# Kernel tuning notes

Hardware: AMD Instinct MI355X
Metric: run time of the kernel (lower is better)

The kernel has to match this reference:

```python
import jax, jax.numpy as jnp
import numpy as np

N_NODES = 50000
N_EDGES = 800000
D = 128


def setup_inputs() -> dict:
    key = jax.random.key(0)
    k1, k2, k3, k4, k5 = jax.random.split(key, 5)
    feature = jax.random.normal(k1, (N_NODES, D), dtype=jnp.float32)
    src = jax.random.randint(k2, (N_EDGES,), 0, N_NODES, dtype=jnp.int64)
    dst = jax.random.randint(k3, (N_EDGES,), 0, N_NODES, dtype=jnp.int64)
    # Linear(in_feats=128, out_feats=128) params
    W = jax.random.normal(k4, (D, D), dtype=jnp.float32) * (1.0 / np.sqrt(D))
    b = jax.random.normal(k5, (D,), dtype=jnp.float32) * 0.01
    return {"feature": feature, "src": src, "dst": dst, "W": W, "b": b}


def reference(feature, src, dst, W, b):
    n = feature.shape[0]
    # copy_src message: each edge carries h[src]; segment-mean over in-edges at dst
    msgs = feature[src]                                      # [E, D] irregular gather
    summed = jax.ops.segment_sum(msgs, dst, num_segments=n)  # [N, D] scatter-add
    cnt = jax.ops.segment_sum(jnp.ones((src.shape[0],), dtype=feature.dtype),
                              dst, num_segments=n)           # in-degree per node
    h = summed / jnp.clip(cnt, 1.0)[:, None]                 # mean (isolated nodes -> 0)
    # NodeApplyModule: ReLU(W h + b)
    return jax.nn.relu(h @ W.T + b)
```

## Files before the change

### kernel.cpp

```cpp
#include <hip/hip_runtime.h>

#define NN 50000
#define NE 800000
#define DD 128
#define NPAD 50176


__global__ __launch_bounds__(256) void k_hist(const int* __restrict__ dst,
                                              int* __restrict__ cnt) {
  int e = blockIdx.x * 256 + threadIdx.x;
  if (e < NE) atomicAdd(&cnt[dst[e]], 1);
}

__global__ __launch_bounds__(1024) void k_scan1(const int* __restrict__ cnt,
                                                int* __restrict__ pos) {
  __shared__ int sh[1024];
  int t = threadIdx.x;
  int base = t * 49;
  int ssum = 0;
  for (int i = 0; i < 49; ++i) ssum += cnt[base + i];
  sh[t] = ssum;
  __syncthreads();
  for (int o = 1; o < 1024; o <<= 1) {
    int x = (t >= o) ? sh[t - o] : 0;
    __syncthreads();
    sh[t] += x;
    __syncthreads();
  }
  int run = sh[t] - ssum;
  for (int i = 0; i < 49; ++i) {
    int v = cnt[base + i];
    pos[base + i] = run;
    run += v;
  }
}

__global__ __launch_bounds__(256) void k_fill(const int* __restrict__ src,
                                              const int* __restrict__ dst,
                                              int* __restrict__ pos,
                                              int* __restrict__ csr) {
  int e = blockIdx.x * 256 + threadIdx.x;
  if (e < NE) {
    int d = dst[e];
    int p = atomicAdd(&pos[d], 1);
    csr[p] = src[e];
  }
}

#define FMA8(R, H)                                          \
  {                                                         \
    acc[R][0] += (H)*w0.x; acc[R][1] += (H)*w0.y;           \
    acc[R][2] += (H)*w0.z; acc[R][3] += (H)*w0.w;           \
    acc[R][4] += (H)*w1.x; acc[R][5] += (H)*w1.y;           \
    acc[R][6] += (H)*w1.z; acc[R][7] += (H)*w1.w;           \
  }

__global__ __launch_bounds__(256) void k_gemmT(const float* __restrict__ feat,
                                               const float* __restrict__ W,
                                               float* __restrict__ g) {
  __shared__ float fs[32][260];
  __shared__ float ws[32][132];
  int tid = threadIdx.x;
  int row0 = blockIdx.x * 256;
  int tc = tid & 15;
  int tr = tid >> 4;
  float acc[16][8] = {};

  for (int kc = 0; kc < 4; ++kc) {
    if (kc) __syncthreads();
    for (int i = 0; i < 8; ++i) {
      int fidx = tid + (i << 8);
      int r = fidx >> 3;
      int q = fidx & 7;
      int grow = row0 + r;
      float4 v = make_float4(0.f, 0.f, 0.f, 0.f);
      if (grow < NN) v = ((const float4*)feat)[grow * 32 + kc * 8 + q];
      int k = q << 2;
      fs[k + 0][r] = v.x;
      fs[k + 1][r] = v.y;
      fs[k + 2][r] = v.z;
      fs[k + 3][r] = v.w;
    }
    for (int i = 0; i < 4; ++i) {
      int fidx = tid + (i << 8);
      int c = fidx >> 3;
      int q = fidx & 7;
      float4 v = ((const float4*)W)[c * 32 + kc * 8 + q];
      int k = q << 2;
      ws[k + 0][c] = v.x;
      ws[k + 1][c] = v.y;
      ws[k + 2][c] = v.z;
      ws[k + 3][c] = v.w;
    }
    __syncthreads();

#pragma unroll 8
    for (int k = 0; k < 32; ++k) {
      float4 w0 = *(const float4*)&ws[k][tc * 8];
      float4 w1 = *(const float4*)&ws[k][tc * 8 + 4];
      float4 h0 = *(const float4*)&fs[k][tr * 16];
      float4 h1 = *(const float4*)&fs[k][tr * 16 + 4];
      float4 h2 = *(const float4*)&fs[k][tr * 16 + 8];
      float4 h3 = *(const float4*)&fs[k][tr * 16 + 12];
      FMA8(0, h0.x) FMA8(1, h0.y) FMA8(2, h0.z) FMA8(3, h0.w)
      FMA8(4, h1.x) FMA8(5, h1.y) FMA8(6, h1.z) FMA8(7, h1.w)
      FMA8(8, h2.x) FMA8(9, h2.y) FMA8(10, h2.z) FMA8(11, h2.w)
      FMA8(12, h3.x) FMA8(13, h3.y) FMA8(14, h3.z) FMA8(15, h3.w)
    }
  }

#pragma unroll
  for (int r = 0; r < 16; ++r) {
    int grow = row0 + tr * 16 + r;
    if (grow < NN) {
      float4 o0, o1;
      o0.x = acc[r][0]; o0.y = acc[r][1]; o0.z = acc[r][2]; o0.w = acc[r][3];
      o1.x = acc[r][4]; o1.y = acc[r][5]; o1.z = acc[r][6]; o1.w = acc[r][7];
      float4* gp = (float4*)(g + (long long)grow * DD) + tc * 2;
      gp[0] = o0;
      gp[1] = o1;
    }
  }
}

__global__ __launch_bounds__(256) void k_gmean(const float* __restrict__ g,
                                               const int* __restrict__ csr,
                                               const int* __restrict__ pos,
                                               const int* __restrict__ cnt,
                                               const float* __restrict__ bias,
                                               float* __restrict__ out) {
  int n = blockIdx.x * 4 + (threadIdx.x >> 6);
  int lane = threadIdx.x & 63;
  int half = lane >> 5;
  int l32 = lane & 31;
  int end = pos[n];
  int c = cnt[n];
  float4 a = make_float4(0.f, 0.f, 0.f, 0.f);
  for (int base = end - c; base < end; base += 64) {
    int m = end - base;
    if (m > 64) m = 64;
    int s = (base + lane < end) ? csr[base + lane] : 0;
    for (int j = 0; j < m; j += 8) {
#pragma unroll
      for (int u = 0; u < 4; ++u) {
        int j2 = j + 2 * u + half;
        int sj = __shfl(s, j2);
        if (j2 < m) {
          float4 v = ((const float4*)(g + (long long)sj * DD))[l32];
          a.x += v.x; a.y += v.y; a.z += v.z; a.w += v.w;
        }
      }
    }
  }
  a.x += __shfl_xor(a.x, 32);
  a.y += __shfl_xor(a.y, 32);
  a.z += __shfl_xor(a.z, 32);
  a.w += __shfl_xor(a.w, 32);
  if (half == 0) {
    float inv = 1.0f / fmaxf((float)c, 1.0f);
    float4 b4 = ((const float4*)bias)[l32];
    float4 o;
    o.x = fmaxf(a.x * inv + b4.x, 0.f);
    o.y = fmaxf(a.y * inv + b4.y, 0.f);
    o.z = fmaxf(a.z * inv + b4.z, 0.f);
    o.w = fmaxf(a.w * inv + b4.w, 0.f);
    ((float4*)(out + (long long)n * DD))[l32] = o;
  }
}

__global__ __launch_bounds__(256) void k_gather_sum(const float* __restrict__ feat,
                                                    const int* __restrict__ csr,
                                                    const int* __restrict__ pos,
                                                    const int* __restrict__ cnt,
                                                    float* __restrict__ sum) {
  int n = blockIdx.x * 4 + (threadIdx.x >> 6);
  int lane = threadIdx.x & 63;
  int end = pos[n];
  int c = cnt[n];
  float ax = 0.f, ay = 0.f;
  for (int base = end - c; base < end; base += 64) {
    int m = end - base;
    if (m > 64) m = 64;
    int s = (base + lane < end) ? csr[base + lane] : 0;
    int j = 0;
    for (; j + 3 < m; j += 4) {
      int s0 = __shfl(s, j), s1 = __shfl(s, j + 1);
      int s2 = __shfl(s, j + 2), s3 = __shfl(s, j + 3);
      float2 v0 = ((const float2*)(feat + (long long)s0 * DD))[lane];
      float2 v1 = ((const float2*)(feat + (long long)s1 * DD))[lane];
      float2 v2 = ((const float2*)(feat + (long long)s2 * DD))[lane];
      float2 v3 = ((const float2*)(feat + (long long)s3 * DD))[lane];
      ax += (v0.x + v1.x) + (v2.x + v3.x);
      ay += (v0.y + v1.y) + (v2.y + v3.y);
    }
    for (; j < m; ++j) {
      int sj = __shfl(s, j);
      float2 v = ((const float2*)(feat + (long long)sj * DD))[lane];
      ax += v.x;
      ay += v.y;
    }
  }
  float2 o;
  o.x = ax;
  o.y = ay;
  ((float2*)(sum + (long long)n * DD))[lane] = o;
}

__global__ __launch_bounds__(256) void k_gemm_inplace(float* __restrict__ io,
                                                      const int* __restrict__ cnt,
                                                      const float* __restrict__ W,
                                                      const float* __restrict__ bias) {
  __shared__ float Wt[64][132];
  __shared__ __attribute__((aligned(16))) float hs[64][72];
  int tid = threadIdx.x;
  int row0 = blockIdx.x * 64;
  int tc = tid & 31;
  int tr = tid >> 5;
  float acc[8][4] = {};
  for (int p = 0; p < 2; ++p) {
    if (p) __syncthreads();
    for (int i = 0; i < 8; ++i) {
      int fidx = tid + (i << 8);
      int c = fidx >> 4;
      int kq = fidx & 15;
      float4 w = ((const float4*)W)[c * 32 + p * 16 + kq];
      int kk = kq << 2;
      Wt[kk + 0][c ^ (((kk + 0) & 31) << 2)] = w.x;
      Wt[kk + 1][c ^ (((kk + 1) & 31) << 2)] = w.y;
      Wt[kk + 2][c ^ (((kk + 2) & 31) << 2)] = w.z;
      Wt[kk + 3][c ^ (((kk + 3) & 31) << 2)] = w.w;
    }
    for (int i = 0; i < 4; ++i) {
      int fidx = tid + (i << 8);
      int r = fidx & 63;
      int kq = fidx >> 6;
      int grow = row0 + r;
      float4 v = make_float4(0.f, 0.f, 0.f, 0.f);
      if (grow < NN) {
        v = ((const float4*)io)[(long long)grow * 32 + p * 16 + kq];
        float inv = 1.0f / fmaxf((float)cnt[grow], 1.0f);
        v.x *= inv; v.y *= inv; v.z *= inv; v.w *= inv;
      }
      int kk = kq << 2;
      hs[kk + 0][r] = v.x;
      hs[kk + 1][r] = v.y;
      hs[kk + 2][r] = v.z;
      hs[kk + 3][r] = v.w;
    }
    __syncthreads();
#pragma unroll 4
    for (int kk = 0; kk < 64; ++kk) {
      float4 w4 = *(const float4*)&Wt[kk][(tc << 2) ^ ((kk & 31) << 2)];
      float4 h0 = *(const float4*)&hs[kk][tr << 3];
      float4 h1 = *(const float4*)&hs[kk][(tr << 3) + 4];
      acc[0][0] += h0.x * w4.x; acc[0][1] += h0.x * w4.y; acc[0][2] += h0.x * w4.z; acc[0][3] += h0.x * w4.w;
      acc[1][0] += h0.y * w4.x; acc[1][1] += h0.y * w4.y; acc[1][2] += h0.y * w4.z; acc[1][3] += h0.y * w4.w;
      acc[2][0] += h0.z * w4.x; acc[2][1] += h0.z * w4.y; acc[2][2] += h0.z * w4.z; acc[2][3] += h0.z * w4.w;
      acc[3][0] += h0.w * w4.x; acc[3][1] += h0.w * w4.y; acc[3][2] += h0.w * w4.z; acc[3][3] += h0.w * w4.w;
      acc[4][0] += h1.x * w4.x; acc[4][1] += h1.x * w4.y; acc[4][2] += h1.x * w4.z; acc[4][3] += h1.x * w4.w;
      acc[5][0] += h1.y * w4.x; acc[5][1] += h1.y * w4.y; acc[5][2] += h1.y * w4.z; acc[5][3] += h1.y * w4.w;
      acc[6][0] += h1.z * w4.x; acc[6][1] += h1.z * w4.y; acc[6][2] += h1.z * w4.z; acc[6][3] += h1.z * w4.w;
      acc[7][0] += h1.w * w4.x; acc[7][1] += h1.w * w4.y; acc[7][2] += h1.w * w4.z; acc[7][3] += h1.w * w4.w;
    }
  }
  float4 b4 = ((const float4*)bias)[tc];
#pragma unroll
  for (int r = 0; r < 8; ++r) {
    int row = row0 + (tr << 3) + r;
    if (row < NN) {
      float4 o;
      o.x = fmaxf(acc[r][0] + b4.x, 0.f);
      o.y = fmaxf(acc[r][1] + b4.y, 0.f);
      o.z = fmaxf(acc[r][2] + b4.z, 0.f);
      o.w = fmaxf(acc[r][3] + b4.w, 0.f);
      ((float4*)(io + (long long)row * DD))[tc] = o;
    }
  }
}

extern "C" void kernel_launch(void* const* d_in, const int* in_sizes, int n_in,
                              void* d_out, int out_size, void* d_ws, size_t ws_size,
                              hipStream_t stream) {
  const float* feature = (const float*)d_in[0];
  const int*   src     = (const int*)d_in[1];
  const int*   dst     = (const int*)d_in[2];
  const float* W       = (const float*)d_in[3];
  const float* bias    = (const float*)d_in[4];
  float* out = (float*)d_out;

  int* cnt = (int*)d_ws;
  int* pos = cnt + NPAD;
  int* csr = pos + NPAD;
  float* g = (float*)(csr + NE);

  size_t need_csr = (size_t)(2 * NPAD + NE) * sizeof(int);
  size_t need_g = need_csr + (size_t)NN * DD * sizeof(float);
  int nblk_e = (NE + 255) / 256;

  hipMemsetAsync(cnt, 0, NPAD * sizeof(int), stream);
  hipLaunchKernelGGL(k_hist, dim3(nblk_e), dim3(256), 0, stream, dst, cnt);
  hipLaunchKernelGGL(k_scan1, dim3(1), dim3(1024), 0, stream, cnt, pos);
  hipLaunchKernelGGL(k_fill, dim3(nblk_e), dim3(256), 0, stream, src, dst, pos, csr);

  if (ws_size >= need_g) {
    hipLaunchKernelGGL(k_gemmT, dim3((NN + 255) / 256), dim3(256), 0, stream,
                       feature, W, g);
    hipLaunchKernelGGL(k_gmean, dim3(NN / 4), dim3(256), 0, stream,
                       g, csr, pos, cnt, bias, out);
  } else {
    hipLaunchKernelGGL(k_gather_sum, dim3(NN / 4), dim3(256), 0, stream,
                       feature, csr, pos, cnt, out);
    hipLaunchKernelGGL(k_gemm_inplace, dim3((NN + 63) / 64), dim3(256), 0,
                       stream, out, cnt, W, bias);
  }
}
```

Baseline: 278.9 us.

## Fuse histogram into GEMM launch, parallelize scan, vectorize fill and gather

Runs the dst histogram in extra blocks of the GEMM launch so both share one kernel, with the GEMM retiled to 128x64 outputs per 128-thread block. The single-block scan becomes a 49-block scan whose block offsets are recomputed in each consumer. The CSR fill now reads int4 vectors of edges, and the gather-mean uses 32-lane half-waves with float4 loads, eight loads in flight and four accumulators. The aim is to remove the serial scan bottleneck and a launch, and to raise memory-level parallelism in the gather. In exchange, every fill and gather block repeats a small prefix over the block sums.

```diff
diff --git a/kernel.cpp b/kernel.cpp
--- a/kernel.cpp
+++ b/kernel.cpp
@@ -4,122 +4,155 @@
 #define NE 800000
 #define DD 128
 #define NPAD 50176
-
-
-__global__ __launch_bounds__(256) void k_hist(const int* __restrict__ dst,
-                                              int* __restrict__ cnt) {
-  int e = blockIdx.x * 256 + threadIdx.x;
-  if (e < NE) atomicAdd(&cnt[dst[e]], 1);
-}
-
-__global__ __launch_bounds__(1024) void k_scan1(const int* __restrict__ cnt,
-                                                int* __restrict__ pos) {
-  __shared__ int sh[1024];
-  int t = threadIdx.x;
-  int base = t * 49;
-  int ssum = 0;
-  for (int i = 0; i < 49; ++i) ssum += cnt[base + i];
-  sh[t] = ssum;
-  __syncthreads();
-  for (int o = 1; o < 1024; o <<= 1) {
-    int x = (t >= o) ? sh[t - o] : 0;
-    __syncthreads();
-    sh[t] += x;
-    __syncthreads();
-  }
-  int run = sh[t] - ssum;
-  for (int i = 0; i < 49; ++i) {
-    int v = cnt[base + i];
-    pos[base + i] = run;
-    run += v;
-  }
-}
-
-__global__ __launch_bounds__(256) void k_fill(const int* __restrict__ src,
-                                              const int* __restrict__ dst,
-                                              int* __restrict__ pos,
-                                              int* __restrict__ csr) {
-  int e = blockIdx.x * 256 + threadIdx.x;
-  if (e < NE) {
-    int d = dst[e];
-    int p = atomicAdd(&pos[d], 1);
-    csr[p] = src[e];
-  }
-}
-
-#define FMA8(R, H)                                          \
-  {                                                         \
-    acc[R][0] += (H)*w0.x; acc[R][1] += (H)*w0.y;           \
-    acc[R][2] += (H)*w0.z; acc[R][3] += (H)*w0.w;           \
-    acc[R][4] += (H)*w1.x; acc[R][5] += (H)*w1.y;           \
-    acc[R][6] += (H)*w1.z; acc[R][7] += (H)*w1.w;           \
-  }
-
-__global__ __launch_bounds__(256) void k_gemmT(const float* __restrict__ feat,
-                                               const float* __restrict__ W,
-                                               float* __restrict__ g) {
-  __shared__ float fs[32][260];
-  __shared__ float ws[32][132];
+#define NSB 49
+#define GB 784
+#define HB 782
+
+
+#define ACC4(A, V) { A.x += V.x; A.y += V.y; A.z += V.z; A.w += V.w; }
+
+#define BSUM_PREFIX(bsum, sbase)                                   \
+  {                                                                \
+    int tt = threadIdx.x;                                          \
+    if (tt < 64) {                                                 \
+      int b = (tt < NSB) ? bsum[tt] : 0;                           \
+      int z = b;                                                   \
+      _Pragma("unroll") for (int o = 1; o < 64; o <<= 1) {         \
+        int w_ = __shfl_up(z, o);                                  \
+        if (tt >= o) z += w_;                                      \
+      }                                                            \
+      sbase[tt] = z - b;                                           \
+    }                                                              \
+    __syncthreads();                                               \
+  }
+
+__global__ __launch_bounds__(128) void k_gemm_hist(
+    const float* __restrict__ feat, const float* __restrict__ W,
+    float* __restrict__ g, const int* __restrict__ dst, int* __restrict__ cnt) {
+  __shared__ float fs[32][132];
+  __shared__ float ws[32][68];
   int tid = threadIdx.x;
-  int row0 = blockIdx.x * 256;
-  int tc = tid & 15;
-  int tr = tid >> 4;
-  float acc[16][8] = {};
+  int bid = blockIdx.x;
+
+  if (bid >= GB) {
+    int idx = (bid - GB) * 128 + tid;
+    if (idx < NE / 8) {
+      const int4* d4 = (const int4*)dst;
+      int4 a = d4[idx * 2];
+      int4 b = d4[idx * 2 + 1];
+      atomicAdd(&cnt[a.x], 1); atomicAdd(&cnt[a.y], 1);
+      atomicAdd(&cnt[a.z], 1); atomicAdd(&cnt[a.w], 1);
+      atomicAdd(&cnt[b.x], 1); atomicAdd(&cnt[b.y], 1);
+      atomicAdd(&cnt[b.z], 1); atomicAdd(&cnt[b.w], 1);
+    }
+    return;
+  }
+
+  int row0 = (bid >> 1) * 128;
+  int col0 = (bid & 1) * 64;
+  int tc = tid & 7;
+  int trb = tid >> 3;
+  int wbase = tc * 8 + ((tc >> 2) << 2);
+  float acc[8][8] = {};
 
   for (int kc = 0; kc < 4; ++kc) {
     if (kc) __syncthreads();
     for (int i = 0; i < 8; ++i) {
-      int fidx = tid + (i << 8);
-      int r = fidx >> 3;
-      int q = fidx & 7;
+      int fidx = tid + (i << 7);
+      int r = fidx >> 3, q = fidx & 7;
       int grow = row0 + r;
       float4 v = make_float4(0.f, 0.f, 0.f, 0.f);
       if (grow < NN) v = ((const float4*)feat)[grow * 32 + kc * 8 + q];
       int k = q << 2;
-      fs[k + 0][r] = v.x;
-      fs[k + 1][r] = v.y;
-      fs[k + 2][r] = v.z;
-      fs[k + 3][r] = v.w;
+      fs[k][r] = v.x; fs[k + 1][r] = v.y; fs[k + 2][r] = v.z; fs[k + 3][r] = v.w;
     }
     for (int i = 0; i < 4; ++i) {
-      int fidx = tid + (i << 8);
-      int c = fidx >> 3;
-      int q = fidx & 7;
-      float4 v = ((const float4*)W)[c * 32 + kc * 8 + q];
+      int fidx = tid + (i << 7);
+      int c = fidx >> 3, q = fidx & 7;
+      float4 v = ((const float4*)W)[(col0 + c) * 32 + kc * 8 + q];
+      int sc = c + ((c >> 5) << 2);
       int k = q << 2;
-      ws[k + 0][c] = v.x;
-      ws[k + 1][c] = v.y;
-      ws[k + 2][c] = v.z;
-      ws[k + 3][c] = v.w;
+      ws[k][sc] = v.x; ws[k + 1][sc] = v.y; ws[k + 2][sc] = v.z; ws[k + 3][sc] = v.w;
     }
     __syncthreads();
+
+#define FM8(R, H)                                                       \
+    { acc[R][0] += (H)*w0.x; acc[R][1] += (H)*w0.y;                     \
+      acc[R][2] += (H)*w0.z; acc[R][3] += (H)*w0.w;                     \
+      acc[R][4] += (H)*w1.x; acc[R][5] += (H)*w1.y;                     \
+      acc[R][6] += (H)*w1.z; acc[R][7] += (H)*w1.w; }
 
 #pragma unroll 8
     for (int k = 0; k < 32; ++k) {
-      float4 w0 = *(const float4*)&ws[k][tc * 8];
-      float4 w1 = *(const float4*)&ws[k][tc * 8 + 4];
-      float4 h0 = *(const float4*)&fs[k][tr * 16];
-      float4 h1 = *(const float4*)&fs[k][tr * 16 + 4];
-      float4 h2 = *(const float4*)&fs[k][tr * 16 + 8];
-      float4 h3 = *(const float4*)&fs[k][tr * 16 + 12];
-      FMA8(0, h0.x) FMA8(1, h0.y) FMA8(2, h0.z) FMA8(3, h0.w)
-      FMA8(4, h1.x) FMA8(5, h1.y) FMA8(6, h1.z) FMA8(7, h1.w)
-      FMA8(8, h2.x) FMA8(9, h2.y) FMA8(10, h2.z) FMA8(11, h2.w)
-      FMA8(12, h3.x) FMA8(13, h3.y) FMA8(14, h3.z) FMA8(15, h3.w)
+      float4 w0 = *(const float4*)&ws[k][wbase];
+      float4 w1 = *(const float4*)&ws[k][wbase + 4];
+      float4 h0 = *(const float4*)&fs[k][trb * 8];
+      float4 h1 = *(const float4*)&fs[k][trb * 8 + 4];
+      FM8(0, h0.x) FM8(1, h0.y) FM8(2, h0.z) FM8(3, h0.w)
+      FM8(4, h1.x) FM8(5, h1.y) FM8(6, h1.z) FM8(7, h1.w)
     }
   }
 
 #pragma unroll
-  for (int r = 0; r < 16; ++r) {
-    int grow = row0 + tr * 16 + r;
+  for (int r = 0; r < 8; ++r) {
+    int grow = row0 + trb * 8 + r;
     if (grow < NN) {
       float4 o0, o1;
       o0.x = acc[r][0]; o0.y = acc[r][1]; o0.z = acc[r][2]; o0.w = acc[r][3];
       o1.x = acc[r][4]; o1.y = acc[r][5]; o1.z = acc[r][6]; o1.w = acc[r][7];
-      float4* gp = (float4*)(g + (long long)grow * DD) + tc * 2;
+      float4* gp = (float4*)(g + (size_t)grow * DD + col0) + tc * 2;
       gp[0] = o0;
       gp[1] = o1;
     }
+  }
+}
+
+__global__ __launch_bounds__(1024) void k_scan(const int* __restrict__ cnt,
+                                               int* __restrict__ pos,
+                                               int* __restrict__ bsum) {
+  __shared__ int wsum[16];
+  int t = threadIdx.x;
+  int gidx = blockIdx.x * 1024 + t;
+  int v = cnt[gidx];
+  int x = v;
+#pragma unroll
+  for (int o = 1; o < 64; o <<= 1) {
+    int y = __shfl_up(x, o);
+    if ((t & 63) >= o) x += y;
+  }
+  if ((t & 63) == 63) wsum[t >> 6] = x;
+  __syncthreads();
+  if (t < 64) {
+    int y = (t < 16) ? wsum[t] : 0;
+    int z = y;
+#pragma unroll
+    for (int o = 1; o < 16; o <<= 1) {
+      int w = __shfl_up(z, o);
+      if (t >= o) z += w;
+    }
+    if (t < 16) wsum[t] = z - y;
+  }
+  __syncthreads();
+  pos[gidx] = wsum[t >> 6] + x - v;
+  if (t == 1023) bsum[blockIdx.x] = wsum[15] + x;
+}
+
+__global__ __launch_bounds__(256) void k_fill(const int* __restrict__ src,
+                                              const int* __restrict__ dst,
+                                              int* __restrict__ pos,
+                                              int* __restrict__ csr,
+                                              const int* __restrict__ bsum) {
+  __shared__ int sbase[64];
+  BSUM_PREFIX(bsum, sbase)
+  int idx = blockIdx.x * 256 + threadIdx.x;
+  if (idx < NE / 4) {
+    int4 d = ((const int4*)dst)[idx];
+    int4 s = ((const int4*)src)[idx];
+    int p;
+    p = atomicAdd(&pos[d.x], 1); csr[sbase[d.x >> 10] + p] = s.x;
+    p = atomicAdd(&pos[d.y], 1); csr[sbase[d.y >> 10] + p] = s.y;
+    p = atomicAdd(&pos[d.z], 1); csr[sbase[d.z >> 10] + p] = s.z;
+    p = atomicAdd(&pos[d.w], 1); csr[sbase[d.w >> 10] + p] = s.w;
   }
 }
 
@@ -127,83 +160,101 @@
                                                const int* __restrict__ csr,
                                                const int* __restrict__ pos,
                                                const int* __restrict__ cnt,
+                                               const int* __restrict__ bsum,
                                                const float* __restrict__ bias,
                                                float* __restrict__ out) {
-  int n = blockIdx.x * 4 + (threadIdx.x >> 6);
-  int lane = threadIdx.x & 63;
-  int half = lane >> 5;
-  int l32 = lane & 31;
-  int end = pos[n];
+  __shared__ int sbase[64];
+  BSUM_PREFIX(bsum, sbase)
+  int tid = threadIdx.x;
+  int hw = tid >> 5, l32 = tid & 31;
+  int n = blockIdx.x * 8 + hw;
   int c = cnt[n];
-  float4 a = make_float4(0.f, 0.f, 0.f, 0.f);
-  for (int base = end - c; base < end; base += 64) {
-    int m = end - base;
-    if (m > 64) m = 64;
-    int s = (base + lane < end) ? csr[base + lane] : 0;
-    for (int j = 0; j < m; j += 8) {
-#pragma unroll
-      for (int u = 0; u < 4; ++u) {
-        int j2 = j + 2 * u + half;
-        int sj = __shfl(s, j2);
-        if (j2 < m) {
-          float4 v = ((const float4*)(g + (long long)sj * DD))[l32];
-          a.x += v.x; a.y += v.y; a.z += v.z; a.w += v.w;
-        }
-      }
-    }
-  }
-  a.x += __shfl_xor(a.x, 32);
-  a.y += __shfl_xor(a.y, 32);
-  a.z += __shfl_xor(a.z, 32);
-  a.w += __shfl_xor(a.w, 32);
-  if (half == 0) {
-    float inv = 1.0f / fmaxf((float)c, 1.0f);
-    float4 b4 = ((const float4*)bias)[l32];
-    float4 o;
-    o.x = fmaxf(a.x * inv + b4.x, 0.f);
-    o.y = fmaxf(a.y * inv + b4.y, 0.f);
-    o.z = fmaxf(a.z * inv + b4.z, 0.f);
-    o.w = fmaxf(a.w * inv + b4.w, 0.f);
-    ((float4*)(out + (long long)n * DD))[l32] = o;
-  }
-}
-
-__global__ __launch_bounds__(256) void k_gather_sum(const float* __restrict__ feat,
-                                                    const int* __restrict__ csr,
-                                                    const int* __restrict__ pos,
-                                                    const int* __restrict__ cnt,
-                                                    float* __restrict__ sum) {
-  int n = blockIdx.x * 4 + (threadIdx.x >> 6);
-  int lane = threadIdx.x & 63;
-  int end = pos[n];
+  int endg = sbase[n >> 10] + pos[n];
+  int start = endg - c;
+  float4 a0 = make_float4(0.f, 0.f, 0.f, 0.f), a1 = a0, a2 = a0, a3 = a0;
+
+  for (int base = start; base < endg; base += 32) {
+    int m = endg - base;
+    if (m > 32) m = 32;
+    int s = (l32 < m) ? csr[base + l32] : 0;
+    int j = 0;
+    for (; j + 8 <= m; j += 8) {
+      int s0 = __shfl(s, j + 0, 32), s1 = __shfl(s, j + 1, 32),
+          s2 = __shfl(s, j + 2, 32), s3 = __shfl(s, j + 3, 32),
+          s4 = __shfl(s, j + 4, 32), s5 = __shfl(s, j + 5, 32),
+          s6 = __shfl(s, j + 6, 32), s7 = __shfl(s, j + 7, 32);
+      float4 v0 = ((const float4*)(g + (size_t)s0 * DD))[l32];
+      float4 v1 = ((const float4*)(g + (size_t)s1 * DD))[l32];
+      float4 v2 = ((const float4*)(g + (size_t)s2 * DD))[l32];
+      float4 v3 = ((const float4*)(g + (size_t)s3 * DD))[l32];
+      float4 v4 = ((const float4*)(g + (size_t)s4 * DD))[l32];
+      float4 v5 = ((const float4*)(g + (size_t)s5 * DD))[l32];
+      float4 v6 = ((const float4*)(g + (size_t)s6 * DD))[l32];
+      float4 v7 = ((const float4*)(g + (size_t)s7 * DD))[l32];
+      ACC4(a0, v0) ACC4(a1, v1) ACC4(a2, v2) ACC4(a3, v3)
+      ACC4(a0, v4) ACC4(a1, v5) ACC4(a2, v6) ACC4(a3, v7)
+    }
+    for (; j < m; ++j) {
+      int sj = __shfl(s, j, 32);
+      float4 v = ((const float4*)(g + (size_t)sj * DD))[l32];
+      ACC4(a0, v)
+    }
+  }
+  a0.x += a1.x + a2.x + a3.x;
+  a0.y += a1.y + a2.y + a3.y;
+  a0.z += a1.z + a2.z + a3.z;
+  a0.w += a1.w + a2.w + a3.w;
+  float inv = 1.0f / fmaxf((float)c, 1.0f);
+  float4 b4 = ((const float4*)bias)[l32];
+  float4 o;
+  o.x = fmaxf(a0.x * inv + b4.x, 0.f);
+  o.y = fmaxf(a0.y * inv + b4.y, 0.f);
+  o.z = fmaxf(a0.z * inv + b4.z, 0.f);
+  o.w = fmaxf(a0.w * inv + b4.w, 0.f);
+  ((float4*)(out + (size_t)n * DD))[l32] = o;
+}
+
+__global__ __launch_bounds__(128) void k_hist(const int* __restrict__ dst,
+                                              int* __restrict__ cnt) {
+  int idx = blockIdx.x * 128 + threadIdx.x;
+  if (idx < NE / 8) {
+    const int4* d4 = (const int4*)dst;
+    int4 a = d4[idx * 2];
+    int4 b = d4[idx * 2 + 1];
+    atomicAdd(&cnt[a.x], 1); atomicAdd(&cnt[a.y], 1);
+    atomicAdd(&cnt[a.z], 1); atomicAdd(&cnt[a.w], 1);
+    atomicAdd(&cnt[b.x], 1); atomicAdd(&cnt[b.y], 1);
+    atomicAdd(&cnt[b.z], 1); atomicAdd(&cnt[b.w], 1);
+  }
+}
+
+__global__ __launch_bounds__(256) void k_gsum(const float* __restrict__ feat,
+                                              const int* __restrict__ csr,
+                                              const int* __restrict__ pos,
+                                              const int* __restrict__ cnt,
+                                              const int* __restrict__ bsum,
+                                              float* __restrict__ out) {
+  __shared__ int sbase[64];
+  BSUM_PREFIX(bsum, sbase)
+  int tid = threadIdx.x;
+  int hw = tid >> 5, l32 = tid & 31;
+  int n = blockIdx.x * 8 + hw;
   int c = cnt[n];
-  float ax = 0.f, ay = 0.f;
-  for (int base = end - c; base < end; base += 64) {
-    int m = end - base;
-    if (m > 64) m = 64;
-    int s = (base + lane < end) ? csr[base + lane] : 0;
-    int j = 0;
-    for (; j + 3 < m; j += 4) {
-      int s0 = __shfl(s, j), s1 = __shfl(s, j + 1);
-      int s2 = __shfl(s, j + 2), s3 = __shfl(s, j + 3);
-      float2 v0 = ((const float2*)(feat + (long long)s0 * DD))[lane];
-      float2 v1 = ((const float2*)(feat + (long long)s1 * DD))[lane];
-      float2 v2 = ((const float2*)(feat + (long long)s2 * DD))[lane];
-      float2 v3 = ((const float2*)(feat + (long long)s3 * DD))[lane];
-      ax += (v0.x + v1.x) + (v2.x + v3.x);
-      ay += (v0.y + v1.y) + (v2.y + v3.y);
-    }
-    for (; j < m; ++j) {
-      int sj = __shfl(s, j);
-      float2 v = ((const float2*)(feat + (long long)sj * DD))[lane];
-      ax += v.x;
-      ay += v.y;
-    }
-  }
-  float2 o;
-  o.x = ax;
-  o.y = ay;
-  ((float2*)(sum + (long long)n * DD))[lane] = o;
+  int endg = sbase[n >> 10] + pos[n];
+  int start = endg - c;
+  float4 a0 = make_float4(0.f, 0.f, 0.f, 0.f), a1 = a0;
+  for (int base = start; base < endg; base += 32) {
+    int m = endg - base;
+    if (m > 32) m = 32;
+    int s = (l32 < m) ? csr[base + l32] : 0;
+    for (int j = 0; j < m; ++j) {
+      int sj = __shfl(s, j, 32);
+      float4 v = ((const float4*)(feat + (size_t)sj * DD))[l32];
+      if (j & 1) { ACC4(a1, v) } else { ACC4(a0, v) }
+    }
+  }
+  a0.x += a1.x; a0.y += a1.y; a0.z += a1.z; a0.w += a1.w;
+  ((float4*)(out + (size_t)n * DD))[l32] = a0;
 }
 
 __global__ __launch_bounds__(256) void k_gemm_inplace(float* __restrict__ io,
@@ -237,7 +288,7 @@
       int grow = row0 + r;
       float4 v = make_float4(0.f, 0.f, 0.f, 0.f);
       if (grow < NN) {
-        v = ((const float4*)io)[(long long)grow * 32 + p * 16 + kq];
+        v = ((const float4*)io)[(size_t)grow * 32 + p * 16 + kq];
         float inv = 1.0f / fmaxf((float)cnt[grow], 1.0f);
         v.x *= inv; v.y *= inv; v.z *= inv; v.w *= inv;
       }
@@ -273,7 +324,7 @@
       o.y = fmaxf(acc[r][1] + b4.y, 0.f);
       o.z = fmaxf(acc[r][2] + b4.z, 0.f);
       o.w = fmaxf(acc[r][3] + b4.w, 0.f);
-      ((float4*)(io + (long long)row * DD))[tc] = o;
+      ((float4*)(io + (size_t)row * DD))[tc] = o;
     }
   }
 }
@@ -288,28 +339,31 @@
   const float* bias    = (const float*)d_in[4];
   float* out = (float*)d_out;
 
-  int* cnt = (int*)d_ws;
-  int* pos = cnt + NPAD;
-  int* csr = pos + NPAD;
-  float* g = (float*)(csr + NE);
-
-  size_t need_csr = (size_t)(2 * NPAD + NE) * sizeof(int);
-  size_t need_g = need_csr + (size_t)NN * DD * sizeof(float);
-  int nblk_e = (NE + 255) / 256;
+  int* cnt  = (int*)d_ws;
+  int* pos  = cnt + NPAD;
+  int* bsum = pos + NPAD;
+  int* csr  = bsum + 64;
+  float* g  = (float*)(csr + NE);
+
+  size_t need_main = (size_t)(2 * NPAD + 64 + NE) * 4 + (size_t)NN * DD * 4;
 
   hipMemsetAsync(cnt, 0, NPAD * sizeof(int), stream);
-  hipLaunchKernelGGL(k_hist, dim3(nblk_e), dim3(256), 0, stream, dst, cnt);
-  hipLaunchKernelGGL(k_scan1, dim3(1), dim3(1024), 0, stream, cnt, pos);
-  hipLaunchKernelGGL(k_fill, dim3(nblk_e), dim3(256), 0, stream, src, dst, pos, csr);
-
-  if (ws_size >= need_g) {
-    hipLaunchKernelGGL(k_gemmT, dim3((NN + 255) / 256), dim3(256), 0, stream,
-                       feature, W, g);
-    hipLaunchKernelGGL(k_gmean, dim3(NN / 4), dim3(256), 0, stream,
-                       g, csr, pos, cnt, bias, out);
+
+  if (ws_size >= need_main) {
+    hipLaunchKernelGGL(k_gemm_hist, dim3(GB + HB), dim3(128), 0, stream,
+                       feature, W, g, dst, cnt);
+    hipLaunchKernelGGL(k_scan, dim3(NSB), dim3(1024), 0, stream, cnt, pos, bsum);
+    hipLaunchKernelGGL(k_fill, dim3((NE / 4 + 255) / 256), dim3(256), 0, stream,
+                       src, dst, pos, csr, bsum);
+    hipLaunchKernelGGL(k_gmean, dim3(NN / 8), dim3(256), 0, stream,
+                       g, csr, pos, cnt, bsum, bias, out);
   } else {
-    hipLaunchKernelGGL(k_gather_sum, dim3(NN / 4), dim3(256), 0, stream,
-                       feature, csr, pos, cnt, out);
+    hipLaunchKernelGGL(k_hist, dim3(HB), dim3(128), 0, stream, dst, cnt);
+    hipLaunchKernelGGL(k_scan, dim3(NSB), dim3(1024), 0, stream, cnt, pos, bsum);
+    hipLaunchKernelGGL(k_fill, dim3((NE / 4 + 255) / 256), dim3(256), 0, stream,
+                       src, dst, pos, csr, bsum);
+    hipLaunchKernelGGL(k_gsum, dim3(NN / 8), dim3(256), 0, stream,
+                       feature, csr, pos, cnt, bsum, out);
     hipLaunchKernelGGL(k_gemm_inplace, dim3((NN + 63) / 64), dim3(256), 0,
                        stream, out, cnt, W, bias);
   }
```

Result: faster. 252.0 us (-9.6%).
